# Optimization experiments

Measured on AMD Instinct MI355X. Metric: run time of the kernel, lower is better.

Reference implementation:

```python
import jax, jax.numpy as jnp
import numpy as np

N_NODES = 100000
N_EDGES = 1600000
NODE_DIM = 128
EDGE_DIM = 64
HID = 64
N_POSTS = 10000


def _gru_cell(x, h, w_ih, w_hh, b_ih, b_hh):
    # torch.nn.GRUCell semantics
    gi = x @ w_ih.T + b_ih          # [N, 3H]
    gh = h @ w_hh.T + b_hh          # [N, 3H]
    i_r, i_z, i_n = jnp.split(gi, 3, axis=-1)
    h_r, h_z, h_n = jnp.split(gh, 3, axis=-1)
    r = jax.nn.sigmoid(i_r + h_r)
    z = jax.nn.sigmoid(i_z + h_z)
    n = jnp.tanh(i_n + r * h_n)
    return (1.0 - z) * n + z * h


def setup_inputs() -> dict:
    key = jax.random.key(0)
    ks = jax.random.split(key, 20)
    s = 0.05
    f32 = jnp.float32
    return {
        "node_features": jax.random.normal(ks[0], (N_NODES, NODE_DIM), dtype=f32),
        "edge_attr": jax.random.normal(ks[1], (N_EDGES, EDGE_DIM), dtype=f32),
        "edge_index": jax.random.randint(ks[2], (2, N_EDGES), 0, N_NODES),
        "post_mask": jax.random.randint(ks[3], (N_POSTS,), 0, N_NODES),
        "n_layers": 2,
        # node_encoder
        "W_node": jax.random.normal(ks[4], (HID, NODE_DIM), dtype=f32) * s,
        "b_node": jnp.zeros((HID,), dtype=f32),
        # edge_encoder
        "W_edge": jax.random.normal(ks[5], (HID, EDGE_DIM), dtype=f32) * s,
        "b_edge": jnp.zeros((HID,), dtype=f32),
        # message_aggregator: Linear(2H -> H)
        "W_agg": jax.random.normal(ks[6], (HID, 2 * HID), dtype=f32) * s,
        "b_agg": jnp.zeros((HID,), dtype=f32),
        # GRUCell(H, H)
        "w_ih": jax.random.normal(ks[7], (3 * HID, HID), dtype=f32) * s,
        "w_hh": jax.random.normal(ks[8], (3 * HID, HID), dtype=f32) * s,
        "b_ih": jnp.zeros((3 * HID,), dtype=f32),
        "b_hh": jnp.zeros((3 * HID,), dtype=f32),
        # output MLP: H -> H//2 -> 1
        "W_out1": jax.random.normal(ks[9], (HID // 2, HID), dtype=f32) * s,
        "b_out1": jnp.zeros((HID // 2,), dtype=f32),
        "W_out2": jax.random.normal(ks[10], (1, HID // 2), dtype=f32) * s,
        "b_out2": jnp.zeros((1,), dtype=f32),
    }


def reference(node_features, edge_attr, edge_index, post_mask, n_layers,
              W_node, b_node, W_edge, b_edge, W_agg, b_agg,
              w_ih, w_hh, b_ih, b_hh, W_out1, b_out1, W_out2, b_out2):
    h = jax.nn.relu(node_features @ W_node.T + b_node)       # [N, H]
    e = jax.nn.relu(edge_attr @ W_edge.T + b_edge)           # [E, H]
    src, dst = edge_index[0], edge_index[1]
    for _ in range(int(n_layers)):
        # batched gather-concat-linear (replaces per-edge python loop)
        msg = jnp.concatenate([h[src], e], axis=1) @ W_agg.T + b_agg  # [E, H]
        messages = jax.ops.segment_sum(msg, dst, num_segments=N_NODES)  # scatter-add
        h = _gru_cell(messages, h, w_ih, w_hh, b_ih, b_hh)
    p = h[post_mask]                                          # [P, H]
    logits = (jax.nn.relu(p @ W_out1.T + b_out1) @ W_out2.T + b_out2).squeeze(-1)
    return jax.nn.sigmoid(logits)
```

## Files before the change

### kernel.cpp

```cpp
#include <hip/hip_runtime.h>

using short8  = __attribute__((ext_vector_type(8))) short;
using ushort8 = __attribute__((ext_vector_type(8))) unsigned short;
using f32x4   = __attribute__((ext_vector_type(4))) float;

static __device__ __forceinline__ short f2bf(float f) {
  unsigned u = __float_as_uint(f);
  u += 0x7fffu + ((u >> 16) & 1u);
  return (short)(u >> 16);
}
static __device__ __forceinline__ float bf2f(short s) {
  return __uint_as_float(((unsigned)(unsigned short)s) << 16);
}
static __device__ __forceinline__ float us2f(unsigned short s) {
  return __uint_as_float(((unsigned)s) << 16);
}
static __device__ __forceinline__ short8 load8_bf16(const float* __restrict__ p) {
  const f32x4* q = (const f32x4*)p;
  f32x4 a = q[0], b = q[1];
  short8 r;
  r[0]=f2bf(a[0]); r[1]=f2bf(a[1]); r[2]=f2bf(a[2]); r[3]=f2bf(a[3]);
  r[4]=f2bf(b[0]); r[5]=f2bf(b[1]); r[6]=f2bf(b[2]); r[7]=f2bf(b[3]);
  return r;
}
static __device__ __forceinline__ void split8(const float* p, short8& hi, short8& lo) {
  const f32x4* q = (const f32x4*)p;
  f32x4 a = q[0], b = q[1];
  float v[8] = {a[0],a[1],a[2],a[3],b[0],b[1],b[2],b[3]};
#pragma unroll
  for (int j = 0; j < 8; ++j) {
    short h = f2bf(v[j]);
    hi[j] = h;
    lo[j] = f2bf(v[j] - bf2f(h));
  }
}

__global__ __launch_bounds__(256) void node_encode(
    const float* __restrict__ X, const float* __restrict__ Wn,
    const float* __restrict__ bn, float* __restrict__ h,
    unsigned short* __restrict__ hb, int nNodes) {
  int tid = threadIdx.x, lane = tid & 63, w = tid >> 6, lg = lane >> 4, lr = lane & 15;
  short8 bf[4][4];
#pragma unroll
  for (int t = 0; t < 4; ++t)
#pragma unroll
    for (int kk = 0; kk < 4; ++kk)
      bf[t][kk] = load8_bf16(Wn + (t*16+lr)*128 + kk*32 + lg*8);
  float bias[4];
#pragma unroll
  for (int t = 0; t < 4; ++t) bias[t] = bn[t*16+lr];

  int base = blockIdx.x * 64 + w * 16;
  int arow = base + lr;
  int nn = arow < nNodes ? arow : nNodes - 1;
  f32x4 acc[4] = {};
#pragma unroll
  for (int kk = 0; kk < 4; ++kk) {
    short8 aH, aL;
    split8(X + (size_t)nn*128 + kk*32 + lg*8, aH, aL);
#pragma unroll
    for (int t = 0; t < 4; ++t) {
      acc[t] = __builtin_amdgcn_mfma_f32_16x16x32_bf16(aH, bf[t][kk], acc[t], 0, 0, 0);
      acc[t] = __builtin_amdgcn_mfma_f32_16x16x32_bf16(aL, bf[t][kk], acc[t], 0, 0, 0);
    }
  }
#pragma unroll
  for (int t = 0; t < 4; ++t)
#pragma unroll
    for (int i = 0; i < 4; ++i) {
      int orow = base + lg*4 + i;
      if (orow < nNodes) {
        float v = fmaxf(acc[t][i] + bias[t], 0.f);
        h[(size_t)orow*64 + t*16 + lr] = v;
        hb[(size_t)orow*64 + t*16 + lr] = (unsigned short)f2bf(v);
      }
    }
}

__global__ __launch_bounds__(256) void hist_deg(
    const int* __restrict__ dst, int* __restrict__ deg, int nEdges) {
  for (int e = blockIdx.x*256 + threadIdx.x; e < nEdges; e += gridDim.x*256)
    atomicAdd(&deg[dst[e]], 1);
}

__global__ __launch_bounds__(256) void scan_pass1(
    const int* __restrict__ deg, int* __restrict__ bsum, int n) {
  int b = blockIdx.x, tid = threadIdx.x;
  int base = b * 4096;
  int s = 0;
  for (int j = tid; j < 4096; j += 256) {
    int i = base + j;
    s += (i < n) ? deg[i] : 0;
  }
  __shared__ int ws[4];
#pragma unroll
  for (int o = 32; o; o >>= 1) s += __shfl_down(s, o);
  if ((tid & 63) == 0) ws[tid >> 6] = s;
  __syncthreads();
  if (tid == 0) bsum[b] = ws[0] + ws[1] + ws[2] + ws[3];
}

__global__ void scan_pass2(const int* __restrict__ bsum, int* __restrict__ boff,
                           int* __restrict__ off, int nBlocks, int n) {
  if (threadIdx.x == 0 && blockIdx.x == 0) {
    int run = 0;
    for (int b = 0; b < nBlocks; ++b) { boff[b] = run; run += bsum[b]; }
    off[n] = run;
  }
}

__global__ __launch_bounds__(256) void scan_pass3(
    const int* __restrict__ deg, const int* __restrict__ boff,
    int* __restrict__ off, int n) {
  int b = blockIdx.x, tid = threadIdx.x;
  int lane = tid & 63, w = tid >> 6;
  int base = b * 4096 + tid * 16;
  int d[16], tot = 0;
#pragma unroll
  for (int j = 0; j < 16; ++j) {
    d[j] = (base + j < n) ? deg[base + j] : 0;
    tot += d[j];
  }
  int s = tot;
#pragma unroll
  for (int o = 1; o < 64; o <<= 1) {
    int t = __shfl_up(s, o);
    if (lane >= o) s += t;
  }
  __shared__ int ws[4];
  if (lane == 63) ws[w] = s;
  __syncthreads();
  int wo = 0;
  for (int k = 0; k < 4; ++k) wo += (k < w) ? ws[k] : 0;
  int run = boff[b] + wo + s - tot;
#pragma unroll
  for (int j = 0; j < 16; ++j) {
    if (base + j < n) off[base + j] = run;
    run += d[j];
  }
}

__global__ __launch_bounds__(256) void fill_csr(
    const int* __restrict__ src, const int* __restrict__ dst,
    const int* __restrict__ off, int* __restrict__ cursor,
    int2* __restrict__ ep, int nEdges) {
  for (int e = blockIdx.x*256 + threadIdx.x; e < nEdges; e += gridDim.x*256) {
    int d = dst[e];
    int pos = off[d] + atomicAdd(&cursor[d], 1);
    int2 v; v.x = e; v.y = src[e];
    ep[pos] = v;
  }
}

#define ETILE 128
__global__ __launch_bounds__(256) void tile_nlo_k(
    const int* __restrict__ off, int* __restrict__ tnlo, int nNodes, int nTiles) {
  int t = blockIdx.x*256 + threadIdx.x;
  if (t > nTiles) return;
  int e0 = t * ETILE;
  int lo = 0, hi = nNodes - 1;
  while (lo < hi) { int m = (lo + hi) >> 1; if (off[m+1] > e0) hi = m; else lo = m + 1; }
  tnlo[t] = lo;
}

__global__ __launch_bounds__(256) void edge_encode_fused(
    const float* __restrict__ EA, const float* __restrict__ We,
    const float* __restrict__ be, const int* __restrict__ off,
    const int2* __restrict__ ep, const int* __restrict__ tnlo,
    float* __restrict__ Esum, int nNodes, int nEdges) {
  __shared__ float tile[ETILE][66];
  int tid = threadIdx.x, lane = tid & 63, w = tid >> 6;
  int lr = lane & 15, lg = lane >> 4;

  short8 bf[4][2];
#pragma unroll
  for (int t = 0; t < 4; ++t)
#pragma unroll
    for (int kk = 0; kk < 2; ++kk)
      bf[t][kk] = load8_bf16(We + (t*16+lr)*64 + kk*32 + lg*8);
  float bias[4];
#pragma unroll
  for (int t = 0; t < 4; ++t) bias[t] = be[t*16+lr];

  int e0 = blockIdx.x * ETILE;
  int e1 = e0 + ETILE; if (e1 > nEdges) e1 = nEdges;
  int er0 = e0 + w*32 + lr;
  int er1 = er0 + 16;
  int ei0 = ep[er0 < nEdges ? er0 : nEdges-1].x;
  int ei1 = ep[er1 < nEdges ? er1 : nEdges-1].x;
  const float* r0p = EA + (size_t)ei0*64;
  const float* r1p = EA + (size_t)ei1*64;
  short8 aH[2][2], aL[2][2];
#pragma unroll
  for (int kk = 0; kk < 2; ++kk) {
    split8(r0p + kk*32 + lg*8, aH[0][kk], aL[0][kk]);
    split8(r1p + kk*32 + lg*8, aH[1][kk], aL[1][kk]);
  }
  f32x4 acc[2][4] = {};
#pragma unroll
  for (int b = 0; b < 2; ++b)
#pragma unroll
    for (int kk = 0; kk < 2; ++kk)
#pragma unroll
      for (int t = 0; t < 4; ++t) {
        acc[b][t] = __builtin_amdgcn_mfma_f32_16x16x32_bf16(aH[b][kk], bf[t][kk], acc[b][t], 0,0,0);
        acc[b][t] = __builtin_amdgcn_mfma_f32_16x16x32_bf16(aL[b][kk], bf[t][kk], acc[b][t], 0,0,0);
      }
#pragma unroll
  for (int b = 0; b < 2; ++b)
#pragma unroll
    for (int t = 0; t < 4; ++t)
#pragma unroll
      for (int i = 0; i < 4; ++i)
        tile[w*32 + b*16 + lg*4 + i][t*16 + lr] = fmaxf(acc[b][t][i] + bias[t], 0.f);
  __syncthreads();

  int nlo = tnlo[blockIdx.x], nhi = tnlo[blockIdx.x + 1];
  for (int n = nlo + w; n <= nhi; n += 4) {
    int a = off[n], b2 = off[n+1];
    int ra = (a > e0 ? a : e0) - e0;
    int rb = (b2 < e1 ? b2 : e1) - e0;
    float s = 0.f;
    int r = ra;
    for (; r + 4 <= rb; r += 4)
      s += tile[r][lane] + tile[r+1][lane] + tile[r+2][lane] + tile[r+3][lane];
    for (; r < rb; ++r) s += tile[r][lane];
    bool interior = (a >= e0) && (b2 <= e1);
    float* p = &Esum[(size_t)n*64 + lane];
    if (interior) *p = s;
    else if (rb > ra) atomicAdd(p, s);
  }
}

__global__ __launch_bounds__(256) void make_combos(
    const float* __restrict__ wih, const float* __restrict__ Wagg,
    const float* __restrict__ bagg, const float* __restrict__ whh,
    short* __restrict__ WceH, short* __restrict__ WceL,
    short* __restrict__ WchH, short* __restrict__ WchL,
    short* __restrict__ whhH, short* __restrict__ whhL, float* __restrict__ bihA) {
  int idx = blockIdx.x*256 + threadIdx.x;
  if (idx < 12288) {
    int r = idx >> 6, k = idx & 63;
    float a = 0.f, b = 0.f;
    for (int j = 0; j < 64; ++j) {
      float ww = wih[r*64 + j];
      a += ww * Wagg[j*128 + k];
      b += ww * Wagg[j*128 + 64 + k];
    }
    short ah = f2bf(a);
    WchH[idx] = ah; WchL[idx] = f2bf(a - bf2f(ah));
    short bh = f2bf(b);
    WceH[idx] = bh; WceL[idx] = f2bf(b - bf2f(bh));
    float wv = whh[idx];
    short hh = f2bf(wv);
    whhH[idx] = hh; whhL[idx] = f2bf(wv - bf2f(hh));
    if (idx < 192) {
      float s = 0.f;
      for (int j = 0; j < 64; ++j) s += wih[idx*64 + j] * bagg[j];
      bihA[idx] = s;
    }
  }
}

__global__ __launch_bounds__(256) void gather_G(
    const unsigned short* __restrict__ hb, const int* __restrict__ off,
    const int2* __restrict__ ep, float* __restrict__ G, int nNodes) {
  int tid = threadIdx.x, lane = tid & 63, w = tid >> 6;
  int er = lane >> 3, fs = lane & 7;
  int n0 = (blockIdx.x * 4 + w) * 4;
  if (n0 >= nNodes) return;
  int a[4], b[4];
#pragma unroll
  for (int j = 0; j < 4; ++j) {
    int n = n0 + j;
    a[j] = (n < nNodes) ? off[n] : 0;
    b[j] = (n < nNodes) ? off[n + 1] : 0;
  }
  float acc[4][8];
#pragma unroll
  for (int j = 0; j < 4; ++j)
#pragma unroll
    for (int q = 0; q < 8; ++q) acc[j][q] = 0.f;
  int mx = 0;
#pragma unroll
  for (int j = 0; j < 4; ++j) { int c = b[j] - a[j]; if (c > mx) mx = c; }
  for (int t = 0; t < mx; t += 8) {
#pragma unroll
    for (int j = 0; j < 4; ++j) {
      int idx = a[j] + t;
      int rem = b[j] - idx;
      if (rem > 0) {
        int e = idx + (er < rem ? er : rem - 1);
        int s = ep[e].y;
        ushort8 v = *(const ushort8*)(hb + (size_t)s * 64 + fs * 8);
        if (er < rem) {
#pragma unroll
          for (int q = 0; q < 8; ++q) acc[j][q] += us2f(v[q]);
        }
      }
    }
  }
#pragma unroll
  for (int j = 0; j < 4; ++j)
#pragma unroll
    for (int q = 0; q < 8; ++q) {
      float v = acc[j][q];
      v += __shfl_xor(v, 8);
      v += __shfl_xor(v, 16);
      v += __shfl_xor(v, 32);
      acc[j][q] = v;
    }
  if (er == 0) {
#pragma unroll
    for (int j = 0; j < 4; ++j) {
      int n = n0 + j;
      if (n < nNodes) {
        f32x4 lo = {acc[j][0], acc[j][1], acc[j][2], acc[j][3]};
        f32x4 hi = {acc[j][4], acc[j][5], acc[j][6], acc[j][7]};
        *(f32x4*)(G + (size_t)n * 64 + fs * 8) = lo;
        *(f32x4*)(G + (size_t)n * 64 + fs * 8 + 4) = hi;
      }
    }
  }
}

__global__ __launch_bounds__(256) void layer_dense(
    const float* __restrict__ h_old, const float* __restrict__ Esum,
    const float* __restrict__ G, const int* __restrict__ deg,
    const short* __restrict__ WceH, const short* __restrict__ WceL,
    const short* __restrict__ WchH, const short* __restrict__ WchL,
    const short* __restrict__ whhH, const short* __restrict__ whhL,
    const float* __restrict__ bihA, const float* __restrict__ bih,
    const float* __restrict__ bhh, float* __restrict__ h_new,
    unsigned short* __restrict__ h_newb, int nNodes) {
  int tid = threadIdx.x, lane = tid & 63, w = tid >> 6;
  int lr = lane & 15, lg = lane >> 4;
  int nb = blockIdx.x * 64;

  int arow = nb + w*16 + lr; if (arow >= nNodes) arow = nNodes - 1;
  short8 EsH[2], EsL[2], GHf[2], GLf[2], HH[2], HL[2];
#pragma unroll
  for (int kk = 0; kk < 2; ++kk) {
    split8(Esum + (size_t)arow*64 + kk*32 + lg*8, EsH[kk], EsL[kk]);
    split8(G + (size_t)arow*64 + kk*32 + lg*8, GHf[kk], GLf[kk]);
    split8(h_old + (size_t)arow*64 + kk*32 + lg*8, HH[kk], HL[kk]);
  }

  int row0 = nb + w*16 + lg*4;
  float degv[4];
#pragma unroll
  for (int i = 0; i < 4; ++i) {
    int n = row0 + i;
    degv[i] = (n < nNodes) ? (float)deg[n] : 0.f;
  }

  f32x4 gi[12], gh[12];
#pragma unroll
  for (int ct = 0; ct < 12; ++ct) {
    float bi = bih[ct*16 + lr], ba = bihA[ct*16 + lr], bh = bhh[ct*16 + lr];
#pragma unroll
    for (int i = 0; i < 4; ++i) { gi[ct][i] = bi + degv[i]*ba; gh[ct][i] = bh; }
  }

#pragma unroll
  for (int ct = 0; ct < 12; ++ct) {
    int wb = (ct*16 + lr)*64 + lg*8;
#pragma unroll
    for (int kk = 0; kk < 2; ++kk) {
      int o = wb + kk*32;
      short8 wceh = *(const short8*)(WceH + o);
      short8 wcel = *(const short8*)(WceL + o);
      short8 wchh = *(const short8*)(WchH + o);
      short8 wchl = *(const short8*)(WchL + o);
      short8 whh_h = *(const short8*)(whhH + o);
      short8 whh_l = *(const short8*)(whhL + o);
      gi[ct] = __builtin_amdgcn_mfma_f32_16x16x32_bf16(EsH[kk], wceh, gi[ct], 0,0,0);
      gi[ct] = __builtin_amdgcn_mfma_f32_16x16x32_bf16(EsL[kk], wceh, gi[ct], 0,0,0);
      gi[ct] = __builtin_amdgcn_mfma_f32_16x16x32_bf16(EsH[kk], wcel, gi[ct], 0,0,0);
      gi[ct] = __builtin_amdgcn_mfma_f32_16x16x32_bf16(GHf[kk], wchh, gi[ct], 0,0,0);
      gi[ct] = __builtin_amdgcn_mfma_f32_16x16x32_bf16(GLf[kk], wchh, gi[ct], 0,0,0);
      gi[ct] = __builtin_amdgcn_mfma_f32_16x16x32_bf16(GHf[kk], wchl, gi[ct], 0,0,0);
      gh[ct] = __builtin_amdgcn_mfma_f32_16x16x32_bf16(HH[kk], whh_h, gh[ct], 0,0,0);
      gh[ct] = __builtin_amdgcn_mfma_f32_16x16x32_bf16(HL[kk], whh_h, gh[ct], 0,0,0);
      gh[ct] = __builtin_amdgcn_mfma_f32_16x16x32_bf16(HH[kk], whh_l, gh[ct], 0,0,0);
    }
  }

#pragma unroll
  for (int ct = 0; ct < 4; ++ct)
#pragma unroll
    for (int i = 0; i < 4; ++i) {
      int n = row0 + i;
      if (n < nNodes) {
        int jh = ct*16 + lr;
        float r = 1.f/(1.f + expf(-(gi[ct][i] + gh[ct][i])));
        float z = 1.f/(1.f + expf(-(gi[ct+4][i] + gh[ct+4][i])));
        float nn = tanhf(gi[ct+8][i] + r * gh[ct+8][i]);
        float hv = h_old[(size_t)n*64 + jh];
        float hn = (1.f - z)*nn + z*hv;
        h_new[(size_t)n*64 + jh] = hn;
        h_newb[(size_t)n*64 + jh] = (unsigned short)f2bf(hn);
      }
    }
}

__global__ __launch_bounds__(256) void out_mlp(
    const float* __restrict__ h, const int* __restrict__ pm,
    const float* __restrict__ W1, const float* __restrict__ b1,
    const float* __restrict__ W2, const float* __restrict__ b2,
    float* __restrict__ out, int nPosts) {
  int tid = threadIdx.x;
  int lane = tid & 63;
  int p = blockIdx.x*4 + (tid >> 6);
  if (p >= nPosts) return;
  int n = pm[p];
  float v = h[(size_t)n*64 + lane];
  int row = lane & 31;
  float o = b1[row];
#pragma unroll
  for (int k = 0; k < 64; ++k) {
    float vb = __shfl(v, k);
    o += vb * W1[row*64 + k];
  }
  o = fmaxf(o, 0.f);
  float val = o * W2[row] * 0.5f;
#pragma unroll
  for (int offm = 32; offm > 0; offm >>= 1) val += __shfl_xor(val, offm);
  if (lane == 0) out[p] = 1.f/(1.f + expf(-(val + b2[0])));
}

static inline char* aln(char*& w, size_t bytes) {
  uintptr_t p = ((uintptr_t)w + 255) & ~(uintptr_t)255;
  char* r = (char*)p;
  w = r + bytes;
  return r;
}

extern "C" void kernel_launch(void* const* d_in, const int* in_sizes, int n_in,
                              void* d_out, int out_size, void* d_ws, size_t ws_size,
                              hipStream_t stream) {
  const float* X    = (const float*)d_in[0];
  const float* EA   = (const float*)d_in[1];
  const int*   EI   = (const int*)d_in[2];
  const int*   PM   = (const int*)d_in[3];
  const float* Wn   = (const float*)d_in[5];
  const float* bn   = (const float*)d_in[6];
  const float* We   = (const float*)d_in[7];
  const float* be   = (const float*)d_in[8];
  const float* Wagg = (const float*)d_in[9];
  const float* bagg = (const float*)d_in[10];
  const float* wih  = (const float*)d_in[11];
  const float* whh  = (const float*)d_in[12];
  const float* bih  = (const float*)d_in[13];
  const float* bhh  = (const float*)d_in[14];
  const float* W1   = (const float*)d_in[15];
  const float* b1   = (const float*)d_in[16];
  const float* W2   = (const float*)d_in[17];
  const float* b2   = (const float*)d_in[18];
  float* out = (float*)d_out;

  int nNodes = in_sizes[0] / 128;
  int nEdges = in_sizes[1] / 64;
  int nPosts = in_sizes[3];
  const int* src = EI;
  const int* dst = EI + nEdges;
  int nTiles = (nEdges + ETILE - 1) / ETILE;
  int nSB = (nNodes + 4095) / 4096;

  char* w = (char*)d_ws;
  float* h0   = (float*)aln(w, (size_t)nNodes * 64 * 4);
  float* h1   = (float*)aln(w, (size_t)nNodes * 64 * 4);
  unsigned short* h0b = (unsigned short*)aln(w, (size_t)nNodes * 64 * 2);
  unsigned short* h1b = (unsigned short*)aln(w, (size_t)nNodes * 64 * 2);
  float* Esum = (float*)aln(w, (size_t)nNodes * 64 * 4);
  float* G    = (float*)aln(w, (size_t)nNodes * 64 * 4);
  short* WceH = (short*)aln(w, 12288 * 2);
  short* WceL = (short*)aln(w, 12288 * 2);
  short* WchH = (short*)aln(w, 12288 * 2);
  short* WchL = (short*)aln(w, 12288 * 2);
  short* whhH = (short*)aln(w, 12288 * 2);
  short* whhL = (short*)aln(w, 12288 * 2);
  float* bihA = (float*)aln(w, 192 * 4);
  int*   off  = (int*)aln(w, (size_t)(nNodes + 1) * 4);
  int*   deg  = (int*)aln(w, (size_t)nNodes * 4);
  int*   cur  = (int*)aln(w, (size_t)nNodes * 4);
  int2*  ep   = (int2*)aln(w, (size_t)nEdges * 8);
  int*   tnlo = (int*)aln(w, (size_t)(nTiles + 1) * 4);
  int*   bsum = (int*)aln(w, (size_t)nSB * 4);
  int*   boff = (int*)aln(w, (size_t)nSB * 4);

  hipMemsetAsync(deg, 0, (size_t)nNodes * 4, stream);
  hipMemsetAsync(cur, 0, (size_t)nNodes * 4, stream);
  hipMemsetAsync(Esum, 0, (size_t)nNodes * 64 * 4, stream);

  hist_deg<<<2048, 256, 0, stream>>>(dst, deg, nEdges);
  scan_pass1<<<nSB, 256, 0, stream>>>(deg, bsum, nNodes);
  scan_pass2<<<1, 1, 0, stream>>>(bsum, boff, off, nSB, nNodes);
  scan_pass3<<<nSB, 256, 0, stream>>>(deg, boff, off, nNodes);
  fill_csr<<<2048, 256, 0, stream>>>(src, dst, off, cur, ep, nEdges);
  tile_nlo_k<<<(nTiles + 256) / 256, 256, 0, stream>>>(off, tnlo, nNodes, nTiles);

  node_encode<<<(nNodes + 63) / 64, 256, 0, stream>>>(X, Wn, bn, h0, h0b, nNodes);
  edge_encode_fused<<<nTiles, 256, 0, stream>>>(EA, We, be, off, ep, tnlo, Esum,
                                                nNodes, nEdges);
  make_combos<<<48, 256, 0, stream>>>(wih, Wagg, bagg, whh,
                                      WceH, WceL, WchH, WchL, whhH, whhL, bihA);

  gather_G<<<(nNodes + 15) / 16, 256, 0, stream>>>(h0b, off, ep, G, nNodes);
  layer_dense<<<(nNodes + 63) / 64, 256, 0, stream>>>(
      h0, Esum, G, deg, WceH, WceL, WchH, WchL, whhH, whhL,
      bihA, bih, bhh, h1, h1b, nNodes);
  gather_G<<<(nNodes + 15) / 16, 256, 0, stream>>>(h1b, off, ep, G, nNodes);
  layer_dense<<<(nNodes + 63) / 64, 256, 0, stream>>>(
      h1, Esum, G, deg, WceH, WceL, WchH, WchL, whhH, whhL,
      bihA, bih, bhh, h0, h0b, nNodes);

  out_mlp<<<(nPosts + 3) / 4, 256, 0, stream>>>(h0, PM, W1, b1, W2, b2, out, nPosts);
}
```

Before: 815.0 us.

## Encode edges in input order, scatter bf16 results to CSR slots, segment-sum separately

The edge encoder now reads edge_attr rows in their original order (coalesced) instead of gathering them through the CSR permutation. It writes bf16 encodings to their sorted CSR position, and a separate seg_sum kernel reduces each node's contiguous run. This drops the tile_nlo kernel, the Esum memset and the atomics. The CSR array splits into separate srcs and pos2 int arrays, and gather_G now handles 16 edges per iteration with source indices loaded ahead of the row loads to raise memory-level parallelism. In exchange it adds a 200MB bf16 intermediate write and read, and the edge features are rounded to bf16 before summation, which costs some precision.

```diff
diff --git a/kernel.cpp b/kernel.cpp
--- a/kernel.cpp
+++ b/kernel.cpp
@@ -143,32 +143,20 @@
 __global__ __launch_bounds__(256) void fill_csr(
     const int* __restrict__ src, const int* __restrict__ dst,
     const int* __restrict__ off, int* __restrict__ cursor,
-    int2* __restrict__ ep, int nEdges) {
+    int* __restrict__ srcs, int* __restrict__ pos2, int nEdges) {
   for (int e = blockIdx.x*256 + threadIdx.x; e < nEdges; e += gridDim.x*256) {
     int d = dst[e];
     int pos = off[d] + atomicAdd(&cursor[d], 1);
-    int2 v; v.x = e; v.y = src[e];
-    ep[pos] = v;
-  }
-}
-
-#define ETILE 128
-__global__ __launch_bounds__(256) void tile_nlo_k(
-    const int* __restrict__ off, int* __restrict__ tnlo, int nNodes, int nTiles) {
-  int t = blockIdx.x*256 + threadIdx.x;
-  if (t > nTiles) return;
-  int e0 = t * ETILE;
-  int lo = 0, hi = nNodes - 1;
-  while (lo < hi) { int m = (lo + hi) >> 1; if (off[m+1] > e0) hi = m; else lo = m + 1; }
-  tnlo[t] = lo;
-}
-
-__global__ __launch_bounds__(256) void edge_encode_fused(
+    srcs[pos] = src[e];
+    pos2[e] = pos;
+  }
+}
+
+__global__ __launch_bounds__(256) void edge_mlp(
     const float* __restrict__ EA, const float* __restrict__ We,
-    const float* __restrict__ be, const int* __restrict__ off,
-    const int2* __restrict__ ep, const int* __restrict__ tnlo,
-    float* __restrict__ Esum, int nNodes, int nEdges) {
-  __shared__ float tile[ETILE][66];
+    const float* __restrict__ be, const int* __restrict__ pos2,
+    unsigned short* __restrict__ encb, int nEdges) {
+  __shared__ float tile[128][66];
   int tid = threadIdx.x, lane = tid & 63, w = tid >> 6;
   int lr = lane & 15, lg = lane >> 4;
 
@@ -182,19 +170,17 @@
 #pragma unroll
   for (int t = 0; t < 4; ++t) bias[t] = be[t*16+lr];
 
-  int e0 = blockIdx.x * ETILE;
-  int e1 = e0 + ETILE; if (e1 > nEdges) e1 = nEdges;
-  int er0 = e0 + w*32 + lr;
-  int er1 = er0 + 16;
-  int ei0 = ep[er0 < nEdges ? er0 : nEdges-1].x;
-  int ei1 = ep[er1 < nEdges ? er1 : nEdges-1].x;
-  const float* r0p = EA + (size_t)ei0*64;
-  const float* r1p = EA + (size_t)ei1*64;
+  int e0 = blockIdx.x * 128;
+  int r0 = e0 + w*32 + lr;
+  int c0 = r0 < nEdges ? r0 : nEdges - 1;
+  int c1 = (r0+16) < nEdges ? (r0+16) : nEdges - 1;
+  const float* p0 = EA + (size_t)c0*64;
+  const float* p1 = EA + (size_t)c1*64;
   short8 aH[2][2], aL[2][2];
 #pragma unroll
   for (int kk = 0; kk < 2; ++kk) {
-    split8(r0p + kk*32 + lg*8, aH[0][kk], aL[0][kk]);
-    split8(r1p + kk*32 + lg*8, aH[1][kk], aL[1][kk]);
+    split8(p0 + kk*32 + lg*8, aH[0][kk], aL[0][kk]);
+    split8(p1 + kk*32 + lg*8, aH[1][kk], aL[1][kk]);
   }
   f32x4 acc[2][4] = {};
 #pragma unroll
@@ -213,22 +199,76 @@
 #pragma unroll
       for (int i = 0; i < 4; ++i)
         tile[w*32 + b*16 + lg*4 + i][t*16 + lr] = fmaxf(acc[b][t][i] + bias[t], 0.f);
-  __syncthreads();
-
-  int nlo = tnlo[blockIdx.x], nhi = tnlo[blockIdx.x + 1];
-  for (int n = nlo + w; n <= nhi; n += 4) {
-    int a = off[n], b2 = off[n+1];
-    int ra = (a > e0 ? a : e0) - e0;
-    int rb = (b2 < e1 ? b2 : e1) - e0;
-    float s = 0.f;
-    int r = ra;
-    for (; r + 4 <= rb; r += 4)
-      s += tile[r][lane] + tile[r+1][lane] + tile[r+2][lane] + tile[r+3][lane];
-    for (; r < rb; ++r) s += tile[r][lane];
-    bool interior = (a >= e0) && (b2 <= e1);
-    float* p = &Esum[(size_t)n*64 + lane];
-    if (interior) *p = s;
-    else if (rb > ra) atomicAdd(p, s);
+  int er = lane >> 3, fs = lane & 7;
+#pragma unroll
+  for (int it = 0; it < 4; ++it) {
+    int r = w*32 + it*8 + er;
+    int e = e0 + r;
+    if (e < nEdges) {
+      int p = pos2[e];
+      const float* tp = &tile[r][fs*8];
+      ushort8 v;
+#pragma unroll
+      for (int q = 0; q < 8; ++q) v[q] = (unsigned short)f2bf(tp[q]);
+      *(ushort8*)(encb + (size_t)p*64 + fs*8) = v;
+    }
+  }
+}
+
+__global__ __launch_bounds__(256) void seg_sum(
+    const unsigned short* __restrict__ encb, const int* __restrict__ off,
+    float* __restrict__ Esum, int nNodes) {
+  int tid = threadIdx.x, lane = tid & 63, w = tid >> 6;
+  int er = lane >> 3, fs = lane & 7;
+  int n0 = (blockIdx.x * 4 + w) * 4;
+  if (n0 >= nNodes) return;
+  int a[4], b[4];
+#pragma unroll
+  for (int j = 0; j < 4; ++j) {
+    int n = n0 + j;
+    a[j] = (n < nNodes) ? off[n] : 0;
+    b[j] = (n < nNodes) ? off[n + 1] : 0;
+  }
+  float acc[4][8];
+#pragma unroll
+  for (int j = 0; j < 4; ++j)
+#pragma unroll
+    for (int q = 0; q < 8; ++q) acc[j][q] = 0.f;
+  int mx = 0;
+#pragma unroll
+  for (int j = 0; j < 4; ++j) { int c = b[j] - a[j]; if (c > mx) mx = c; }
+  for (int t = 0; t < mx; t += 8) {
+#pragma unroll
+    for (int j = 0; j < 4; ++j) {
+      int i0 = a[j] + t + er;
+      if (i0 < b[j]) {
+        ushort8 v = *(const ushort8*)(encb + (size_t)i0*64 + fs*8);
+#pragma unroll
+        for (int q = 0; q < 8; ++q) acc[j][q] += us2f(v[q]);
+      }
+    }
+  }
+#pragma unroll
+  for (int j = 0; j < 4; ++j)
+#pragma unroll
+    for (int q = 0; q < 8; ++q) {
+      float v = acc[j][q];
+      v += __shfl_xor(v, 8);
+      v += __shfl_xor(v, 16);
+      v += __shfl_xor(v, 32);
+      acc[j][q] = v;
+    }
+  if (er == 0) {
+#pragma unroll
+    for (int j = 0; j < 4; ++j) {
+      int n = n0 + j;
+      if (n < nNodes) {
+        f32x4 lo = {acc[j][0], acc[j][1], acc[j][2], acc[j][3]};
+        f32x4 hi = {acc[j][4], acc[j][5], acc[j][6], acc[j][7]};
+        *(f32x4*)(Esum + (size_t)n * 64 + fs * 8) = lo;
+        *(f32x4*)(Esum + (size_t)n * 64 + fs * 8 + 4) = hi;
+      }
+    }
   }
 }
 
@@ -264,7 +304,7 @@
 
 __global__ __launch_bounds__(256) void gather_G(
     const unsigned short* __restrict__ hb, const int* __restrict__ off,
-    const int2* __restrict__ ep, float* __restrict__ G, int nNodes) {
+    const int* __restrict__ srcs, float* __restrict__ G, int nNodes) {
   int tid = threadIdx.x, lane = tid & 63, w = tid >> 6;
   int er = lane >> 3, fs = lane & 7;
   int n0 = (blockIdx.x * 4 + w) * 4;
@@ -284,19 +324,30 @@
   int mx = 0;
 #pragma unroll
   for (int j = 0; j < 4; ++j) { int c = b[j] - a[j]; if (c > mx) mx = c; }
-  for (int t = 0; t < mx; t += 8) {
+  for (int t = 0; t < mx; t += 16) {
+    int s0[4], s1[4];
+    bool m0[4], m1[4];
 #pragma unroll
     for (int j = 0; j < 4; ++j) {
-      int idx = a[j] + t;
-      int rem = b[j] - idx;
-      if (rem > 0) {
-        int e = idx + (er < rem ? er : rem - 1);
-        int s = ep[e].y;
-        ushort8 v = *(const ushort8*)(hb + (size_t)s * 64 + fs * 8);
-        if (er < rem) {
-#pragma unroll
-          for (int q = 0; q < 8; ++q) acc[j][q] += us2f(v[q]);
-        }
+      int i0 = a[j] + t + er, i1 = i0 + 8;
+      int bm = b[j] - 1;
+      m0[j] = i0 < b[j]; m1[j] = i1 < b[j];
+      int c0 = m0[j] ? i0 : (bm > a[j] ? bm : a[j]);
+      int c1 = m1[j] ? i1 : c0;
+      s0[j] = (b[j] > a[j]) ? srcs[c0] : 0;
+      s1[j] = (b[j] > a[j]) ? srcs[c1] : 0;
+    }
+#pragma unroll
+    for (int j = 0; j < 4; ++j) {
+      ushort8 v0 = *(const ushort8*)(hb + (size_t)s0[j] * 64 + fs * 8);
+      ushort8 v1 = *(const ushort8*)(hb + (size_t)s1[j] * 64 + fs * 8);
+      if (m0[j]) {
+#pragma unroll
+        for (int q = 0; q < 8; ++q) acc[j][q] += us2f(v0[q]);
+      }
+      if (m1[j]) {
+#pragma unroll
+        for (int q = 0; q < 8; ++q) acc[j][q] += us2f(v1[q]);
       }
     }
   }
@@ -464,7 +515,6 @@
   int nPosts = in_sizes[3];
   const int* src = EI;
   const int* dst = EI + nEdges;
-  int nTiles = (nEdges + ETILE - 1) / ETILE;
   int nSB = (nNodes + 4095) / 4096;
 
   char* w = (char*)d_ws;
@@ -484,33 +534,32 @@
   int*   off  = (int*)aln(w, (size_t)(nNodes + 1) * 4);
   int*   deg  = (int*)aln(w, (size_t)nNodes * 4);
   int*   cur  = (int*)aln(w, (size_t)nNodes * 4);
-  int2*  ep   = (int2*)aln(w, (size_t)nEdges * 8);
-  int*   tnlo = (int*)aln(w, (size_t)(nTiles + 1) * 4);
+  int*   srcs = (int*)aln(w, (size_t)nEdges * 4);
+  int*   pos2 = (int*)aln(w, (size_t)nEdges * 4);
   int*   bsum = (int*)aln(w, (size_t)nSB * 4);
   int*   boff = (int*)aln(w, (size_t)nSB * 4);
+  unsigned short* encb = (unsigned short*)aln(w, (size_t)nEdges * 64 * 2);
 
   hipMemsetAsync(deg, 0, (size_t)nNodes * 4, stream);
   hipMemsetAsync(cur, 0, (size_t)nNodes * 4, stream);
-  hipMemsetAsync(Esum, 0, (size_t)nNodes * 64 * 4, stream);
 
   hist_deg<<<2048, 256, 0, stream>>>(dst, deg, nEdges);
   scan_pass1<<<nSB, 256, 0, stream>>>(deg, bsum, nNodes);
   scan_pass2<<<1, 1, 0, stream>>>(bsum, boff, off, nSB, nNodes);
   scan_pass3<<<nSB, 256, 0, stream>>>(deg, boff, off, nNodes);
-  fill_csr<<<2048, 256, 0, stream>>>(src, dst, off, cur, ep, nEdges);
-  tile_nlo_k<<<(nTiles + 256) / 256, 256, 0, stream>>>(off, tnlo, nNodes, nTiles);
+  fill_csr<<<2048, 256, 0, stream>>>(src, dst, off, cur, srcs, pos2, nEdges);
 
   node_encode<<<(nNodes + 63) / 64, 256, 0, stream>>>(X, Wn, bn, h0, h0b, nNodes);
-  edge_encode_fused<<<nTiles, 256, 0, stream>>>(EA, We, be, off, ep, tnlo, Esum,
-                                                nNodes, nEdges);
+  edge_mlp<<<(nEdges + 127) / 128, 256, 0, stream>>>(EA, We, be, pos2, encb, nEdges);
+  seg_sum<<<(nNodes + 15) / 16, 256, 0, stream>>>(encb, off, Esum, nNodes);
   make_combos<<<48, 256, 0, stream>>>(wih, Wagg, bagg, whh,
                                       WceH, WceL, WchH, WchL, whhH, whhL, bihA);
 
-  gather_G<<<(nNodes + 15) / 16, 256, 0, stream>>>(h0b, off, ep, G, nNodes);
+  gather_G<<<(nNodes + 15) / 16, 256, 0, stream>>>(h0b, off, srcs, G, nNodes);
   layer_dense<<<(nNodes + 63) / 64, 256, 0, stream>>>(
       h0, Esum, G, deg, WceH, WceL, WchH, WchL, whhH, whhL,
       bihA, bih, bhh, h1, h1b, nNodes);
-  gather_G<<<(nNodes + 15) / 16, 256, 0, stream>>>(h1b, off, ep, G, nNodes);
+  gather_G<<<(nNodes + 15) / 16, 256, 0, stream>>>(h1b, off, srcs, G, nNodes);
   layer_dense<<<(nNodes + 63) / 64, 256, 0, stream>>>(
       h1, Esum, G, deg, WceH, WceL, WchH, WchL, whhH, whhL,
       bihA, bih, bhh, h0, h0b, nNodes);
```

New measurement: 865.8 us. 1.06x slower.
